# Optimization experiments

Hardware: AMD Instinct MI355X
Metric: run time of the kernel (lower is better)

Reference implementation:

```python
import jax, jax.numpy as jnp
import numpy as np
from jax import lax

OBS_LEN = 8
PRED_LEN = 12
DIM = 128      # hidden_dim
EMB = 64       # embedding_dim
HEADS = 4
MODES = 5
SCENE = 32     # peds per scene
NPED = 8192    # total peds (256 scenes)


def _lin(key, out_d, in_d):
    kw, kb = jax.random.split(key)
    w = jax.random.normal(kw, (out_d, in_d), jnp.float32) / np.sqrt(in_d).astype(np.float32)
    b = jax.random.normal(kb, (out_d,), jnp.float32) * 0.01
    return w, b


def _stack(key, n, out_d, in_d):
    ws, bs = zip(*[_lin(k, out_d, in_d) for k in jax.random.split(key, n)])
    return jnp.stack(ws), jnp.stack(bs)


def setup_inputs() -> dict:
    key = jax.random.key(0)
    ks = jax.random.split(key, 24)
    inp = {}
    inp['obs_traj'] = jax.random.normal(ks[0], (OBS_LEN, NPED, 2), jnp.float32)
    inp['pe_w'], inp['pe_b'] = _lin(ks[1], EMB, 2)
    inp['lstm_wih'], inp['lstm_bih'] = _lin(ks[2], 4 * DIM, EMB)
    inp['lstm_whh'], inp['lstm_bhh'] = _lin(ks[3], 4 * DIM, DIM)
    inp['rp_w1'], inp['rp_b1'] = _lin(ks[4], DIM // 2, 2)
    inp['rp_w2'], inp['rp_b2'] = _lin(ks[5], DIM, DIM // 2)
    inp['wq'], inp['bq'] = _lin(ks[6], DIM, DIM)
    inp['wk'], inp['bk'] = _lin(ks[7], DIM, DIM)
    inp['wv'], inp['bv'] = _lin(ks[8], DIM, DIM)
    inp['wo'], inp['bo'] = _lin(ks[9], DIM, DIM)
    inp['op_w'], inp['op_b'] = _lin(ks[10], DIM, 2 * DIM)
    inp['mp_w1'], inp['mp_b1'] = _lin(ks[11], DIM, 2 * DIM)
    inp['mp_w2'], inp['mp_b2'] = _lin(ks[12], MODES, DIM)
    inp['td_w1'], inp['td_b1'] = _stack(ks[13], MODES, DIM, 2 * DIM)
    inp['td_w2'], inp['td_b2'] = _stack(ks[14], MODES, DIM, DIM)
    inp['td_w3'], inp['td_b3'] = _stack(ks[15], MODES, PRED_LEN * 2, DIM)
    inp['ud_w1'], inp['ud_b1'] = _stack(ks[16], MODES, DIM // 2, 2 * DIM)
    inp['ud_w2'], inp['ud_b2'] = _stack(ks[17], MODES, PRED_LEN * 2, DIM // 2)
    inp['scene_size'] = SCENE
    return inp


def reference(obs_traj, pe_w, pe_b, lstm_wih, lstm_bih, lstm_whh, lstm_bhh,
              rp_w1, rp_b1, rp_w2, rp_b2, wq, bq, wk, bk, wv, bv, wo, bo,
              op_w, op_b, mp_w1, mp_b1, mp_w2, mp_b2,
              td_w1, td_b1, td_w2, td_b2, td_w3, td_b3,
              ud_w1, ud_b1, ud_w2, ud_b2, scene_size):
    obs = jnp.transpose(obs_traj, (1, 0, 2))          # (N, T, 2)
    N = obs.shape[0]
    D = lstm_whh.shape[1]

    # ---- NodeHistoryEncoder: Linear embed + 1-layer LSTM, last hidden ----
    emb = jnp.einsum('ntd,ed->nte', obs, pe_w) + pe_b  # (N, T, EMB)

    def step(carry, x):
        h, c = carry
        g = x @ lstm_wih.T + lstm_bih + h @ lstm_whh.T + lstm_bhh
        i, f, gg, o = jnp.split(g, 4, axis=-1)          # torch gate order i,f,g,o
        c = jax.nn.sigmoid(f) * c + jax.nn.sigmoid(i) * jnp.tanh(gg)
        h = jax.nn.sigmoid(o) * jnp.tanh(c)
        return (h, c), None

    h0 = jnp.zeros((N, D), obs.dtype)
    (node_features, _), _ = lax.scan(step, (h0, h0), jnp.swapaxes(emb, 0, 1))
    last_pos = obs[:, -1, :]                            # (N, 2)

    # ---- EdgeEncoder: per-scene rel-pos-biased multi-head attention ----
    S = scene_size
    B = N // S
    feat = node_features.reshape(B, S, D)
    pos = last_pos.reshape(B, S, 2)
    rel = pos[:, None, :, :] - pos[:, :, None, :]       # [b,i,j] = pos_j - pos_i
    rel_enc = jax.nn.relu(jnp.einsum('bijd,hd->bijh', rel, rp_w1) + rp_b1)
    rel_enc = jnp.einsum('bijh,eh->bije', rel_enc, rp_w2) + rp_b2  # (B,S,S,D)
    kv = feat[:, None, :, :] + rel_enc                  # key == value
    dh = D // HEADS
    q = (feat @ wq.T + bq).reshape(B, S, HEADS, dh)
    kp = (jnp.einsum('bijd,ed->bije', kv, wk) + bk).reshape(B, S, S, HEADS, dh)
    vp = (jnp.einsum('bijd,ed->bije', kv, wv) + bv).reshape(B, S, S, HEADS, dh)
    scores = jnp.einsum('bihd,bijhd->bhij', q, kp) / np.sqrt(dh).astype(np.float32)
    attn = jax.nn.softmax(scores, axis=-1)
    ctx = jnp.einsum('bhij,bijhd->bihd', attn, vp).reshape(B, S, D)
    attn_out = ctx @ wo.T + bo
    edge = (jnp.concatenate([feat, attn_out], axis=-1) @ op_w.T + op_b).reshape(N, D)

    f_all = jnp.concatenate([node_features, edge], axis=-1)  # (N, 2D)

    # ---- GMMDecoder ----
    probs = jax.nn.softmax(jax.nn.relu(f_all @ mp_w1.T + mp_b1) @ mp_w2.T + mp_b2, axis=-1)
    h1 = jax.nn.relu(jnp.einsum('nd,mhd->nmh', f_all, td_w1) + td_b1)    # (N,M,D)
    h2 = jax.nn.relu(jnp.einsum('nmh,mgh->nmg', h1, td_w2) + td_b2)
    traj = (jnp.einsum('nmg,mog->nmo', h2, td_w3) + td_b3).reshape(N, MODES, PRED_LEN, 2)
    u1 = jax.nn.relu(jnp.einsum('nd,mhd->nmh', f_all, ud_w1) + ud_b1)
    sigmas = jax.nn.softplus(jnp.einsum('nmh,moh->nmo', u1, ud_w2) + ud_b2).reshape(N, MODES, PRED_LEN, 2)
    predictions = jnp.cumsum(traj, axis=2) + last_pos[:, None, None, :]
    return predictions, probs
```

## Files before the change

### kernel.cpp

```cpp
#include <hip/hip_runtime.h>
#include <math.h>

typedef __attribute__((ext_vector_type(8))) short short8;
typedef __attribute__((ext_vector_type(4))) float f32x4;

#define NPED 8192
#define INVS 0.1767766952966369f

#define B_WHH    0
#define B_WQKV   131072
#define B_WK2PAD 229376
#define B_OPWE   294912
#define B_MPW1   360448
#define B_TDW1   425984
#define B_TDW2   753664
#define B_TDW3C  917504
#define F_WIHE   958464
#define F_BEFF   962560
#define F_WV2T   964608
#define F_BQKV   997376
#define F_BEDGE  998912
#define F_TDB3C  999424
#define F_ZERO   999936
#define A_FEAT   1000960
#define A_QKV    3098112

__device__ __forceinline__ float bf2f(ushort u) {
  union { unsigned i; float f; } v; v.i = ((unsigned)u) << 16; return v.f;
}
__device__ __forceinline__ float blo(unsigned u) {
  union { unsigned i; float f; } v; v.i = u << 16; return v.f;
}
__device__ __forceinline__ float bhi(unsigned u) {
  union { unsigned i; float f; } v; v.i = u & 0xffff0000u; return v.f;
}
__device__ __forceinline__ ushort f2bf(float f) {
  union { float f; unsigned i; } v; v.f = f;
  unsigned r = v.i + 0x7fffu + ((v.i >> 16) & 1u);
  return (ushort)(r >> 16);
}

__global__ __launch_bounds__(256) void prep(
    const float* __restrict__ wih, const float* __restrict__ bih, const float* __restrict__ bhh,
    const float* __restrict__ pew, const float* __restrict__ peb,
    const float* __restrict__ wk, const float* __restrict__ wv,
    const float* __restrict__ rpw2, const float* __restrict__ rpb2,
    const float* __restrict__ bq, const float* __restrict__ bk, const float* __restrict__ bv,
    const float* __restrict__ whh, const float* __restrict__ wq, const float* __restrict__ wo,
    const float* __restrict__ opw, const float* __restrict__ opb, const float* __restrict__ bo,
    const float* __restrict__ mpw1,
    const float* __restrict__ tdw1, const float* __restrict__ tdw2,
    const float* __restrict__ tdw3, const float* __restrict__ tdb3,
    char* __restrict__ wsb) {
  int tid = blockIdx.x * 256 + threadIdx.x;
  if (tid < 512) {
    int d = tid;
    float s0 = 0.f, s1 = 0.f, sb = 0.f;
    for (int e = 0; e < 64; ++e) {
      float w = wih[d * 64 + e];
      s0 += w * pew[e * 2]; s1 += w * pew[e * 2 + 1]; sb += w * peb[e];
    }
    ((float*)(wsb + F_WIHE))[d * 2] = s0;
    ((float*)(wsb + F_WIHE))[d * 2 + 1] = s1;
    ((float*)(wsb + F_BEFF))[d] = bih[d] + bhh[d] + sb;
  } else if (tid < 49664) {
    int j = tid - 512; int n = j >> 7, k = j & 127;
    float v = (n < 128) ? wq[n * 128 + k] * INVS
                        : (n < 256) ? wk[(n - 128) * 128 + k] : wv[(n - 256) * 128 + k];
    ((ushort*)(wsb + B_WQKV))[j] = f2bf(v);
  } else if (tid < 82432) {
    int idx = tid - 49664; int r = idx >> 7, d = idx & 127;
    int h = r >> 6, e = r & 63;
    float s = 0.f;
    if ((d >> 5) == h)
      for (int c = 0; c < 128; ++c) s += wk[d * 128 + c] * rpw2[c * 64 + e];
    ((ushort*)(wsb + B_WK2PAD))[idx] = f2bf(s);
  } else if (tid < 115200) {
    int idx = tid - 82432; int o = idx >> 8, k = idx & 255;
    float s;
    if (k < 128) s = opw[o * 256 + k];
    else {
      s = 0.f;
      for (int c = 0; c < 128; ++c) s += opw[o * 256 + 128 + c] * wo[c * 128 + (k - 128)];
    }
    ((ushort*)(wsb + B_OPWE))[idx] = f2bf(s);
  } else if (tid < 147968) {
    int j = tid - 115200; ((ushort*)(wsb + B_MPW1))[j] = f2bf(mpw1[j]);
  } else if (tid < 311808) {
    int j = tid - 147968; ((ushort*)(wsb + B_TDW1))[j] = f2bf(tdw1[j]);
  } else if (tid < 393728) {
    int j = tid - 311808; ((ushort*)(wsb + B_TDW2))[j] = f2bf(tdw2[j]);
  } else if (tid < 414208) {
    int j = tid - 393728; int m = j >> 12, r = j & 4095, o = r >> 7, k = r & 127;
    float s = 0.f;
    if (o < 24) {
      int c = o & 1, jj = o >> 1;
      for (int jp = 0; jp <= jj; ++jp) s += tdw3[(m * 24 + jp * 2 + c) * 128 + k];
    }
    ((ushort*)(wsb + B_TDW3C))[j] = f2bf(s);
  } else if (tid < 414328) {
    int j = tid - 414208; int m = j / 24, o = j % 24;
    int c = o & 1, jj = o >> 1;
    float s = 0.f;
    for (int jp = 0; jp <= jj; ++jp) s += tdb3[m * 24 + jp * 2 + c];
    ((float*)(wsb + F_TDB3C))[j] = s;
  } else if (tid < 414712) {
    int d = tid - 414328;
    float s;
    if (d < 128) s = bq[d] * INVS;
    else if (d < 256) {
      int dd = d - 128; s = bk[dd];
      for (int c = 0; c < 128; ++c) s += wk[dd * 128 + c] * rpb2[c];
    } else {
      int dd = d - 256; s = bv[dd];
      for (int c = 0; c < 128; ++c) s += wv[dd * 128 + c] * rpb2[c];
    }
    ((float*)(wsb + F_BQKV))[d] = s;
  } else if (tid < 414840) {
    int o = tid - 414712;
    float s = opb[o];
    for (int c = 0; c < 128; ++c) s += opw[o * 256 + 128 + c] * bo[c];
    ((float*)(wsb + F_BEDGE))[o] = s;
  } else if (tid < 415096) {
    ((float*)(wsb + F_ZERO))[tid - 414840] = 0.f;
  } else if (tid < 423288) {
    int idx = tid - 415096; int e = idx >> 7, hd = idx & 127;
    float s = 0.f;
    for (int c = 0; c < 128; ++c) s += wv[hd * 128 + c] * rpw2[c * 64 + e];
    ((float*)(wsb + F_WV2T))[idx] = s;
  } else if (tid < 488824) {
    int i = tid - 423288;
    ((ushort*)(wsb + B_WHH))[i] = f2bf(whh[i]);
  }
}

__global__ __launch_bounds__(512) void lstm_mfma(
    const float* __restrict__ obs, const ushort* __restrict__ whhb,
    const float* __restrict__ wihe, const float* __restrict__ beff,
    ushort* __restrict__ feat) {
  __shared__ ushort Hs[32 * 128];
  __shared__ float obs_s[8][32][2];
  int tid = threadIdx.x;
  int w = tid >> 6, l = tid & 63;
  int lm = l & 15, lg = l >> 4;
  int nb = blockIdx.x * 32;
  {
    int ts = tid >> 6, p = (tid >> 1) & 31, c = tid & 1;
    obs_s[ts][p][c] = obs[ts * (NPED * 2) + (nb + p) * 2 + c];
  }
  for (int i = tid; i < 4096; i += 512) Hs[i] = 0;
  short8 bfr[4][4];
  float wx0[4], wx1[4], be[4];
#pragma unroll
  for (int q = 0; q < 4; ++q) {
    int g = q * 128 + w * 16 + lm;
    wx0[q] = wihe[g * 2]; wx1[q] = wihe[g * 2 + 1]; be[q] = beff[g];
#pragma unroll
    for (int ks = 0; ks < 4; ++ks)
      bfr[q][ks] = *(const short8*)(const void*)&whhb[g * 128 + ks * 32 + lg * 8];
  }
  float cst[2][4] = {};
  __syncthreads();
  for (int ts = 0; ts < 8; ++ts) {
    f32x4 acc[2][4];
#pragma unroll
    for (int mi = 0; mi < 2; ++mi)
#pragma unroll
      for (int r = 0; r < 4; ++r) {
        int p = mi * 16 + lg * 4 + r;
        float ox = obs_s[ts][p][0], oy = obs_s[ts][p][1];
#pragma unroll
        for (int q = 0; q < 4; ++q)
          acc[mi][q][r] = be[q] + wx0[q] * ox + wx1[q] * oy;
      }
#pragma unroll
    for (int ks = 0; ks < 4; ++ks) {
      int p0 = lm, p1 = 16 + lm;
      short8 a0 = *(const short8*)(const void*)&Hs[p0 * 128 + ((ks * 32 + lg * 8) ^ ((p0 & 7) << 3))];
      short8 a1 = *(const short8*)(const void*)&Hs[p1 * 128 + ((ks * 32 + lg * 8) ^ ((p1 & 7) << 3))];
#pragma unroll
      for (int q = 0; q < 4; ++q) {
        acc[0][q] = __builtin_amdgcn_mfma_f32_16x16x32_bf16(a0, bfr[q][ks], acc[0][q], 0, 0, 0);
        acc[1][q] = __builtin_amdgcn_mfma_f32_16x16x32_bf16(a1, bfr[q][ks], acc[1][q], 0, 0, 0);
      }
    }
    __syncthreads();
    int d = w * 16 + lm;
#pragma unroll
    for (int mi = 0; mi < 2; ++mi)
#pragma unroll
      for (int r = 0; r < 4; ++r) {
        int p = mi * 16 + lg * 4 + r;
        float xi = acc[mi][0][r], xf = acc[mi][1][r], xg = acc[mi][2][r], xo = acc[mi][3][r];
        float ig = 1.f / (1.f + __expf(-xi));
        float fg = 1.f / (1.f + __expf(-xf));
        xg = fminf(fmaxf(xg, -30.f), 30.f);
        float eg = __expf(-2.f * xg);
        float gg = (1.f - eg) / (1.f + eg);
        float og = 1.f / (1.f + __expf(-xo));
        float cv = fg * cst[mi][r] + ig * gg;
        cst[mi][r] = cv;
        float cvc = fminf(fmaxf(cv, -30.f), 30.f);
        float ec = __expf(-2.f * cvc);
        float th = (1.f - ec) / (1.f + ec);
        ushort hb = f2bf(og * th);
        Hs[p * 128 + (d ^ ((p & 7) << 3))] = hb;
        if (ts == 7) feat[(size_t)(nb + p) * 128 + d] = hb;
      }
    __syncthreads();
  }
}

template<int NF, int NKS, int K1KS>
__global__ __launch_bounds__(256) void mfma_gemm(
    const ushort* __restrict__ A1, int lda1,
    const ushort* __restrict__ A2, int lda2,
    const ushort* __restrict__ Bw,
    const float* __restrict__ bias,
    ushort* __restrict__ out, int ldo, int ooff, int relu) {
  int w = threadIdx.x >> 6, l = threadIdx.x & 63;
  int lm = l & 15, lg = l >> 4;
  int row = blockIdx.x * 64 + w * 16 + lm;
  int col0 = blockIdx.y * (NF * 16);
  f32x4 acc[NF];
#pragma unroll
  for (int i = 0; i < NF; ++i) acc[i] = (f32x4){0.f, 0.f, 0.f, 0.f};
#pragma unroll
  for (int ks = 0; ks < NKS; ++ks) {
    int kb = ks * 32 + lg * 8;
    const ushort* ap = (ks < K1KS) ? (A1 + (size_t)row * lda1 + kb)
                                   : (A2 + (size_t)row * lda2 + (kb - K1KS * 32));
    short8 af = *(const short8*)(const void*)ap;
#pragma unroll
    for (int ni = 0; ni < NF; ++ni) {
      short8 bf = *(const short8*)(const void*)(Bw + (size_t)(col0 + ni * 16 + lm) * (NKS * 32) + kb);
      acc[ni] = __builtin_amdgcn_mfma_f32_16x16x32_bf16(af, bf, acc[ni], 0, 0, 0);
    }
  }
  int orow0 = blockIdx.x * 64 + w * 16 + lg * 4;
#pragma unroll
  for (int ni = 0; ni < NF; ++ni) {
    int c = col0 + ni * 16 + lm;
    float bv = bias[c];
#pragma unroll
    for (int r = 0; r < 4; ++r) {
      float v = acc[ni][r] + bv;
      if (relu) v = fmaxf(v, 0.f);
      out[(size_t)(orow0 + r) * ldo + ooff + c] = f2bf(v);
    }
  }
}

__global__ __launch_bounds__(256) void mp_probs(
    const ushort* __restrict__ feat, const ushort* __restrict__ qkv,
    const ushort* __restrict__ w1b, const float* __restrict__ mpb1,
    const float* __restrict__ mpw2, const float* __restrict__ mpb2,
    float* __restrict__ out) {
  __shared__ float w2s[5][128];
  int t = threadIdx.x;
  for (int i = t; i < 640; i += 256) w2s[i >> 7][i & 127] = mpw2[i];
  __syncthreads();
  int w = t >> 6, l = t & 63, lm = l & 15, lg = l >> 4;
  int row = blockIdx.x * 64 + w * 16 + lm;
  f32x4 acc[8];
#pragma unroll
  for (int i = 0; i < 8; ++i) acc[i] = (f32x4){0.f, 0.f, 0.f, 0.f};
#pragma unroll
  for (int ks = 0; ks < 8; ++ks) {
    int kb = ks * 32 + lg * 8;
    const ushort* ap = (ks < 4) ? (feat + (size_t)row * 128 + kb)
                                : (qkv + (size_t)row * 640 + 256 + (kb - 128));
    short8 af = *(const short8*)(const void*)ap;
#pragma unroll
    for (int ni = 0; ni < 8; ++ni) {
      short8 bf = *(const short8*)(const void*)(w1b + (size_t)(ni * 16 + lm) * 256 + kb);
      acc[ni] = __builtin_amdgcn_mfma_f32_16x16x32_bf16(af, bf, acc[ni], 0, 0, 0);
    }
  }
  float bc[8];
#pragma unroll
  for (int ni = 0; ni < 8; ++ni) bc[ni] = mpb1[ni * 16 + lm];
  float lgt[4][5];
#pragma unroll
  for (int r = 0; r < 4; ++r)
#pragma unroll
    for (int m = 0; m < 5; ++m) {
      float s = 0.f;
#pragma unroll
      for (int ni = 0; ni < 8; ++ni)
        s += fmaxf(acc[ni][r] + bc[ni], 0.f) * w2s[m][ni * 16 + lm];
      lgt[r][m] = s;
    }
#pragma unroll
  for (int mask = 1; mask < 16; mask <<= 1)
#pragma unroll
    for (int r = 0; r < 4; ++r)
#pragma unroll
      for (int m = 0; m < 5; ++m)
        lgt[r][m] += __shfl_xor(lgt[r][m], mask);
  if (lm < 5) {
#pragma unroll
    for (int r = 0; r < 4; ++r) {
      float b0 = lgt[r][0] + mpb2[0];
      float mx = b0;
      float lv[5]; lv[0] = b0;
#pragma unroll
      for (int m = 1; m < 5; ++m) { lv[m] = lgt[r][m] + mpb2[m]; mx = fmaxf(mx, lv[m]); }
      float sm = 0.f;
#pragma unroll
      for (int m = 0; m < 5; ++m) { lv[m] = expf(lv[m] - mx); sm += lv[m]; }
      int n = blockIdx.x * 64 + w * 16 + lg * 4 + r;
      out[983040 + (size_t)n * 5 + lm] = lv[lm] / sm;
    }
  }
}

__global__ __launch_bounds__(256) void td_fused(
    const ushort* __restrict__ feat, const ushort* __restrict__ qkv,
    const ushort* __restrict__ w1b, const float* __restrict__ tdb1,
    const ushort* __restrict__ w2b, const float* __restrict__ tdb2,
    const ushort* __restrict__ w3c, const float* __restrict__ b3c,
    const float* __restrict__ obs, float* __restrict__ out) {
  __shared__ ushort slab[64 * 136];
  int t = threadIdx.x, w = t >> 6, l = t & 63, lm = l & 15, lg = l >> 4;
  int m = blockIdx.y;
  int row = blockIdx.x * 64 + w * 16 + lm;
  const ushort* W1 = w1b + (size_t)m * 32768;
  const ushort* W2 = w2b + (size_t)m * 16384;
  const ushort* W3 = w3c + (size_t)m * 4096;
  const float* B1 = tdb1 + m * 128;
  const float* B2 = tdb2 + m * 128;
  f32x4 a1[8];
#pragma unroll
  for (int i = 0; i < 8; ++i) a1[i] = (f32x4){0.f, 0.f, 0.f, 0.f};
#pragma unroll
  for (int ks = 0; ks < 8; ++ks) {
    int kb = ks * 32 + lg * 8;
    const ushort* ap = (ks < 4) ? (feat + (size_t)row * 128 + kb)
                                : (qkv + (size_t)row * 640 + 256 + (kb - 128));
    short8 af = *(const short8*)(const void*)ap;
#pragma unroll
    for (int ni = 0; ni < 8; ++ni) {
      short8 bf = *(const short8*)(const void*)(W1 + (size_t)(ni * 16 + lm) * 256 + kb);
      a1[ni] = __builtin_amdgcn_mfma_f32_16x16x32_bf16(af, bf, a1[ni], 0, 0, 0);
    }
  }
#pragma unroll
  for (int ni = 0; ni < 8; ++ni) {
    float bb = B1[ni * 16 + lm];
#pragma unroll
    for (int r = 0; r < 4; ++r)
      slab[(w * 16 + lg * 4 + r) * 136 + ni * 16 + lm] = f2bf(fmaxf(a1[ni][r] + bb, 0.f));
  }
  __syncthreads();
  short8 af2[4];
#pragma unroll
  for (int ks = 0; ks < 4; ++ks)
    af2[ks] = *(const short8*)(const void*)&slab[(w * 16 + lm) * 136 + ks * 32 + lg * 8];
  f32x4 a2[8];
#pragma unroll
  for (int i = 0; i < 8; ++i) a2[i] = (f32x4){0.f, 0.f, 0.f, 0.f};
#pragma unroll
  for (int ks = 0; ks < 4; ++ks) {
    int kb = ks * 32 + lg * 8;
#pragma unroll
    for (int ni = 0; ni < 8; ++ni) {
      short8 bf = *(const short8*)(const void*)(W2 + (size_t)(ni * 16 + lm) * 128 + kb);
      a2[ni] = __builtin_amdgcn_mfma_f32_16x16x32_bf16(af2[ks], bf, a2[ni], 0, 0, 0);
    }
  }
  __syncthreads();
#pragma unroll
  for (int ni = 0; ni < 8; ++ni) {
    float bb = B2[ni * 16 + lm];
#pragma unroll
    for (int r = 0; r < 4; ++r)
      slab[(w * 16 + lg * 4 + r) * 136 + ni * 16 + lm] = f2bf(fmaxf(a2[ni][r] + bb, 0.f));
  }
  __syncthreads();
  short8 af3[4];
#pragma unroll
  for (int ks = 0; ks < 4; ++ks)
    af3[ks] = *(const short8*)(const void*)&slab[(w * 16 + lm) * 136 + ks * 32 + lg * 8];
  f32x4 a3[2];
  a3[0] = (f32x4){0.f, 0.f, 0.f, 0.f}; a3[1] = (f32x4){0.f, 0.f, 0.f, 0.f};
#pragma unroll
  for (int ks = 0; ks < 4; ++ks) {
    int kb = ks * 32 + lg * 8;
#pragma unroll
    for (int ni = 0; ni < 2; ++ni) {
      short8 bf = *(const short8*)(const void*)(W3 + (size_t)(ni * 16 + lm) * 128 + kb);
      a3[ni] = __builtin_amdgcn_mfma_f32_16x16x32_bf16(af3[ks], bf, a3[ni], 0, 0, 0);
    }
  }
#pragma unroll
  for (int ni = 0; ni < 2; ++ni) {
    int o = ni * 16 + lm;
    if (o < 24) {
      float bb = b3c[m * 24 + o];
      int c = o & 1;
#pragma unroll
      for (int r = 0; r < 4; ++r) {
        int n = blockIdx.x * 64 + w * 16 + lg * 4 + r;
        out[(size_t)n * 120 + m * 24 + o] = a3[ni][r] + bb + obs[7 * (NPED * 2) + n * 2 + c];
      }
    }
  }
}

__global__ __launch_bounds__(256) void attn_kernel(
    const float* __restrict__ obs, ushort* QKV,
    const float* __restrict__ wv2T,
    const float* __restrict__ rpw1, const float* __restrict__ rpb1) {
  __shared__ ushort K0s[32 * 128];
  __shared__ ushort V0s[32 * 128];
  __shared__ ushort renc[4 * 32 * 64];
  __shared__ float Qi[4][128];
  __shared__ float QWs[4][256];
  __shared__ float att[4][4][32];
  __shared__ float AR[4][4][64];
  __shared__ float rpx[64], rpy[64], rpb[64];
  __shared__ float posS[32][2];
  __shared__ float posI[4][2];
  int t = threadIdx.x;
  int scene = blockIdx.x & 255, ic = blockIdx.x >> 8;
  int i0 = ic * 4, sbase = scene * 32;

  for (int idx = t; idx < 1024; idx += 256) {
    int arr = idx >> 9, j = (idx >> 4) & 31, c = idx & 15;
    short8 v = *(const short8*)(const void*)&QKV[(size_t)(sbase + j) * 640 + 128 + arr * 128 + c * 8];
    ushort* dst = arr ? V0s : K0s;
    *(short8*)(void*)&dst[j * 128 + (c ^ (j & 7)) * 8] = v;
  }
  for (int idx = t; idx < 512; idx += 256) {
    int ii = idx >> 7, d = idx & 127;
    Qi[ii][d] = bf2f(QKV[(size_t)(sbase + i0 + ii) * 640 + d]);
  }
  for (int idx = t; idx < 1024; idx += 256) {
    int ii = idx >> 8, e = idx & 255;
    QWs[ii][e] = bf2f(QKV[(size_t)(sbase + i0 + ii) * 640 + 384 + e]);
  }
  if (t < 64) posS[t >> 1][t & 1] = obs[7 * (NPED * 2) + (sbase + (t >> 1)) * 2 + (t & 1)];
  else if (t < 72) {
    int q = t - 64;
    posI[q >> 1][q & 1] = obs[7 * (NPED * 2) + (sbase + i0 + (q >> 1)) * 2 + (q & 1)];
  } else if (t >= 128 && t < 192) {
    int e = t - 128;
    rpx[e] = rpw1[e * 2]; rpy[e] = rpw1[e * 2 + 1]; rpb[e] = rpb1[e];
  }
  __syncthreads();

  for (int idx = t; idx < 1024; idx += 256) {
    int ii = idx >> 8, j = (idx >> 3) & 31, c = idx & 7;
    float dx = posS[j][0] - posI[ii][0], dy = posS[j][1] - posI[ii][1];
    short8 pk;
#pragma unroll
    for (int r = 0; r < 8; ++r) {
      int e = c * 8 + r;
      pk[r] = (short)f2bf(fmaxf(rpx[e] * dx + rpy[e] * dy + rpb[e], 0.f));
    }
    *(short8*)(void*)&renc[(ii * 32 + j) * 64 + (c ^ (j & 7)) * 8] = pk;
  }
  __syncthreads();

  for (int idx = t; idx < 512; idx += 256) {
    int ii = idx >> 7, h = (idx >> 5) & 3, j = idx & 31;
    float s = 0.f;
#pragma unroll
    for (int cc = 0; cc < 4; ++cc) {
      uint4 kv = *(const uint4*)(const void*)&K0s[j * 128 + (((h * 4 + cc) ^ (j & 7)) * 8)];
      const float4 qa = *(const float4*)&Qi[ii][h * 32 + cc * 8];
      const float4 qb = *(const float4*)&Qi[ii][h * 32 + cc * 8 + 4];
      s += blo(kv.x) * qa.x + bhi(kv.x) * qa.y + blo(kv.y) * qa.z + bhi(kv.y) * qa.w;
      s += blo(kv.z) * qb.x + bhi(kv.z) * qb.y + blo(kv.w) * qb.z + bhi(kv.w) * qb.w;
    }
#pragma unroll
    for (int c = 0; c < 8; ++c) {
      uint4 rv = *(const uint4*)(const void*)&renc[(ii * 32 + j) * 64 + ((c ^ (j & 7)) * 8)];
      const float4 ua = *(const float4*)&QWs[ii][h * 64 + c * 8];
      const float4 ub = *(const float4*)&QWs[ii][h * 64 + c * 8 + 4];
      s += blo(rv.x) * ua.x + bhi(rv.x) * ua.y + blo(rv.y) * ua.z + bhi(rv.y) * ua.w;
      s += blo(rv.z) * ub.x + bhi(rv.z) * ub.y + blo(rv.w) * ub.z + bhi(rv.w) * ub.w;
    }
    att[ii][h][j] = s;
  }
  __syncthreads();

  {
    int r = t >> 4, lj = t & 15;
    float v0 = att[r >> 2][r & 3][lj], v1 = att[r >> 2][r & 3][lj + 16];
    float mx = fmaxf(v0, v1);
    mx = fmaxf(mx, __shfl_xor(mx, 8, 16));
    mx = fmaxf(mx, __shfl_xor(mx, 4, 16));
    mx = fmaxf(mx, __shfl_xor(mx, 2, 16));
    mx = fmaxf(mx, __shfl_xor(mx, 1, 16));
    float e0 = expf(v0 - mx), e1 = expf(v1 - mx);
    float sm = e0 + e1;
    sm += __shfl_xor(sm, 8, 16);
    sm += __shfl_xor(sm, 4, 16);
    sm += __shfl_xor(sm, 2, 16);
    sm += __shfl_xor(sm, 1, 16);
    float inv = 1.f / sm;
    att[r >> 2][r & 3][lj] = e0 * inv;
    att[r >> 2][r & 3][lj + 16] = e1 * inv;
  }
  __syncthreads();

  {
    int ii = t >> 6, h = (t >> 4) & 3, e4 = t & 15;
    int c = e4 >> 1, off = (e4 & 1) * 4;
    float a0 = 0.f, a1 = 0.f, a2 = 0.f, a3 = 0.f;
    for (int j = 0; j < 32; ++j) {
      float av = att[ii][h][j];
      uint2 rv = *(const uint2*)(const void*)&renc[(ii * 32 + j) * 64 + ((c ^ (j & 7)) * 8) + off];
      a0 += av * blo(rv.x); a1 += av * bhi(rv.x);
      a2 += av * blo(rv.y); a3 += av * bhi(rv.y);
    }
    *(float4*)&AR[ii][h][e4 * 4] = make_float4(a0, a1, a2, a3);
  }
  __syncthreads();

  {
    int ii = t >> 6, l = t & 63;
    int h5 = l >> 5, hd4 = l & 31;
    int hd = hd4 * 4, h = hd >> 5;
    float c0 = 0.f, c1 = 0.f, c2 = 0.f, c3 = 0.f;
    int cch = hd >> 3, offh = hd & 7;
    for (int j = h5 * 16; j < h5 * 16 + 16; ++j) {
      float av = att[ii][h][j];
      uint2 vv = *(const uint2*)(const void*)&V0s[j * 128 + ((cch ^ (j & 7)) * 8) + offh];
      c0 += av * blo(vv.x); c1 += av * bhi(vv.x);
      c2 += av * blo(vv.y); c3 += av * bhi(vv.y);
    }
    for (int e4 = h5 * 8; e4 < h5 * 8 + 8; ++e4) {
      const float4 ar = *(const float4*)&AR[ii][h][e4 * 4];
#pragma unroll
      for (int r = 0; r < 4; ++r) {
        const float4 wv = *(const float4*)&wv2T[(e4 * 4 + r) * 128 + hd];
        float a = (r == 0) ? ar.x : (r == 1) ? ar.y : (r == 2) ? ar.z : ar.w;
        c0 += a * wv.x; c1 += a * wv.y; c2 += a * wv.z; c3 += a * wv.w;
      }
    }
    c0 += __shfl_xor(c0, 32); c1 += __shfl_xor(c1, 32);
    c2 += __shfl_xor(c2, 32); c3 += __shfl_xor(c3, 32);
    if (h5 == 0) {
      ushort4 o;
      o.x = f2bf(c0); o.y = f2bf(c1); o.z = f2bf(c2); o.w = f2bf(c3);
      *(ushort4*)(void*)&QKV[(size_t)(sbase + i0 + ii) * 640 + hd] = o;
    }
  }
}

extern "C" void kernel_launch(void* const* d_in, const int* in_sizes, int n_in,
                              void* d_out, int out_size, void* d_ws, size_t ws_size,
                              hipStream_t stream) {
  (void)in_sizes; (void)n_in; (void)out_size; (void)ws_size;
  const float* obs  = (const float*)d_in[0];
  const float* pew  = (const float*)d_in[1];
  const float* peb  = (const float*)d_in[2];
  const float* wih  = (const float*)d_in[3];
  const float* bih  = (const float*)d_in[4];
  const float* whh  = (const float*)d_in[5];
  const float* bhh  = (const float*)d_in[6];
  const float* rpw1 = (const float*)d_in[7];
  const float* rpb1 = (const float*)d_in[8];
  const float* rpw2 = (const float*)d_in[9];
  const float* rpb2 = (const float*)d_in[10];
  const float* wq   = (const float*)d_in[11];
  const float* bq   = (const float*)d_in[12];
  const float* wk   = (const float*)d_in[13];
  const float* bk   = (const float*)d_in[14];
  const float* wv   = (const float*)d_in[15];
  const float* bv   = (const float*)d_in[16];
  const float* wo   = (const float*)d_in[17];
  const float* bo   = (const float*)d_in[18];
  const float* opw  = (const float*)d_in[19];
  const float* opb  = (const float*)d_in[20];
  const float* mpw1 = (const float*)d_in[21];
  const float* mpb1 = (const float*)d_in[22];
  const float* mpw2 = (const float*)d_in[23];
  const float* mpb2 = (const float*)d_in[24];
  const float* tdw1 = (const float*)d_in[25];
  const float* tdb1 = (const float*)d_in[26];
  const float* tdw2 = (const float*)d_in[27];
  const float* tdb2 = (const float*)d_in[28];
  const float* tdw3 = (const float*)d_in[29];
  const float* tdb3 = (const float*)d_in[30];
  char* wsb = (char*)d_ws;
  float* out = (float*)d_out;

  ushort* whhb   = (ushort*)(wsb + B_WHH);
  ushort* wqkvb  = (ushort*)(wsb + B_WQKV);
  ushort* wk2pb  = (ushort*)(wsb + B_WK2PAD);
  ushort* opweb  = (ushort*)(wsb + B_OPWE);
  ushort* mpw1b  = (ushort*)(wsb + B_MPW1);
  ushort* tdw1b  = (ushort*)(wsb + B_TDW1);
  ushort* tdw2b  = (ushort*)(wsb + B_TDW2);
  ushort* tdw3cb = (ushort*)(wsb + B_TDW3C);
  ushort* featb  = (ushort*)(wsb + A_FEAT);
  ushort* qkvb   = (ushort*)(wsb + A_QKV);

  prep<<<1910, 256, 0, stream>>>(wih, bih, bhh, pew, peb, wk, wv, rpw2, rpb2,
                                 bq, bk, bv, whh, wq, wo, opw, opb, bo, mpw1,
                                 tdw1, tdw2, tdw3, tdb3, wsb);
  lstm_mfma<<<256, 512, 0, stream>>>(obs, whhb, (float*)(wsb + F_WIHE),
                                     (float*)(wsb + F_BEFF), featb);
  mfma_gemm<4, 4, 4><<<dim3(128, 6), 256, 0, stream>>>(
      featb, 128, featb, 128, wqkvb, (float*)(wsb + F_BQKV), qkvb, 640, 0, 0);
  mfma_gemm<4, 4, 4><<<dim3(128, 4), 256, 0, stream>>>(
      qkvb, 640, qkvb, 640, wk2pb, (float*)(wsb + F_ZERO), qkvb, 640, 384, 0);
  attn_kernel<<<2048, 256, 0, stream>>>(obs, qkvb, (float*)(wsb + F_WV2T), rpw1, rpb1);
  mfma_gemm<4, 8, 4><<<dim3(128, 2), 256, 0, stream>>>(
      featb, 128, qkvb, 640, opweb, (float*)(wsb + F_BEDGE), qkvb, 640, 256, 0);
  mp_probs<<<128, 256, 0, stream>>>(featb, qkvb, mpw1b, mpb1, mpw2, mpb2, out);
  td_fused<<<dim3(128, 5), 256, 0, stream>>>(featb, qkvb, tdw1b, tdb1, tdw2b, tdb2,
                                             tdw3cb, (float*)(wsb + F_TDB3C), obs, out);
}
```

Baseline: 276.4 us.

## Fold K-projection into QKV weights, fuse mode-prob into trajectory decoder, halve row tiles

New measurement: 265.5 us. 1.04x faster.

```diff
diff --git a/kernel.cpp b/kernel.cpp
--- a/kernel.cpp
+++ b/kernel.cpp
@@ -9,21 +9,20 @@
 
 #define B_WHH    0
 #define B_WQKV   131072
-#define B_WK2PAD 229376
-#define B_OPWE   294912
-#define B_MPW1   360448
-#define B_TDW1   425984
-#define B_TDW2   753664
-#define B_TDW3C  917504
-#define F_WIHE   958464
-#define F_BEFF   962560
-#define F_WV2T   964608
-#define F_BQKV   997376
-#define F_BEDGE  998912
-#define F_TDB3C  999424
-#define F_ZERO   999936
-#define A_FEAT   1000960
-#define A_QKV    3098112
+#define B_WK2PAD 294912
+#define B_OPWE   360448
+#define B_MPW1   425984
+#define B_TDW1   491520
+#define B_TDW2   819200
+#define B_TDW3C  983040
+#define F_WIHE   1024000
+#define F_BEFF   1028096
+#define F_WV2T   1030144
+#define F_BQKV   1062912
+#define F_BEDGE  1065472
+#define F_TDB3C  1065984
+#define A_FEAT   1066496
+#define A_QKV    3163648
 
 __device__ __forceinline__ float bf2f(ushort u) {
   union { unsigned i; float f; } v; v.i = ((unsigned)u) << 16; return v.f;
@@ -104,25 +103,23 @@
     float s = 0.f;
     for (int jp = 0; jp <= jj; ++jp) s += tdb3[m * 24 + jp * 2 + c];
     ((float*)(wsb + F_TDB3C))[j] = s;
-  } else if (tid < 414712) {
+  } else if (tid < 414968) {
     int d = tid - 414328;
-    float s;
+    float s = 0.f;
     if (d < 128) s = bq[d] * INVS;
     else if (d < 256) {
       int dd = d - 128; s = bk[dd];
       for (int c = 0; c < 128; ++c) s += wk[dd * 128 + c] * rpb2[c];
-    } else {
+    } else if (d < 384) {
       int dd = d - 256; s = bv[dd];
       for (int c = 0; c < 128; ++c) s += wv[dd * 128 + c] * rpb2[c];
     }
     ((float*)(wsb + F_BQKV))[d] = s;
-  } else if (tid < 414840) {
-    int o = tid - 414712;
+  } else if (tid < 415096) {
+    int o = tid - 414968;
     float s = opb[o];
     for (int c = 0; c < 128; ++c) s += opw[o * 256 + 128 + c] * bo[c];
     ((float*)(wsb + F_BEDGE))[o] = s;
-  } else if (tid < 415096) {
-    ((float*)(wsb + F_ZERO))[tid - 414840] = 0.f;
   } else if (tid < 423288) {
     int idx = tid - 415096; int e = idx >> 7, hd = idx & 127;
     float s = 0.f;
@@ -131,6 +128,29 @@
   } else if (tid < 488824) {
     int i = tid - 423288;
     ((ushort*)(wsb + B_WHH))[i] = f2bf(whh[i]);
+  }
+}
+
+__global__ __launch_bounds__(256) void prep2(
+    const ushort* __restrict__ wk2pad, const float* __restrict__ wq,
+    const float* __restrict__ bq, ushort* __restrict__ wqkv, float* __restrict__ bqkv) {
+  int idx = blockIdx.x * 256 + threadIdx.x;
+  if (idx < 32768) {
+    int e = idx >> 7, k = idx & 127, h = e >> 6;
+    float s = 0.f;
+    for (int dd = 0; dd < 32; ++dd) {
+      int d = h * 32 + dd;
+      s += bf2f(wk2pad[e * 128 + d]) * wq[d * 128 + k];
+    }
+    wqkv[(384 + e) * 128 + k] = f2bf(s * INVS);
+  } else if (idx < 33024) {
+    int e = idx - 32768, h = e >> 6;
+    float s = 0.f;
+    for (int dd = 0; dd < 32; ++dd) {
+      int d = h * 32 + dd;
+      s += bf2f(wk2pad[e * 128 + d]) * bq[d];
+    }
+    bqkv[384 + e] = s * INVS;
   }
 }
 
@@ -211,7 +231,7 @@
   }
 }
 
-template<int NF, int NKS, int K1KS>
+template<int NF, int NKS, int K1KS, int RS>
 __global__ __launch_bounds__(256) void mfma_gemm(
     const ushort* __restrict__ A1, int lda1,
     const ushort* __restrict__ A2, int lda2,
@@ -220,8 +240,16 @@
     ushort* __restrict__ out, int ldo, int ooff, int relu) {
   int w = threadIdx.x >> 6, l = threadIdx.x & 63;
   int lm = l & 15, lg = l >> 4;
-  int row = blockIdx.x * 64 + w * 16 + lm;
-  int col0 = blockIdx.y * (NF * 16);
+  int row, col0, orow0;
+  if (RS) {
+    row = blockIdx.x * 32 + (w >> 1) * 16 + lm;
+    col0 = blockIdx.y * (NF * 32) + (w & 1) * (NF * 16);
+    orow0 = blockIdx.x * 32 + (w >> 1) * 16 + lg * 4;
+  } else {
+    row = blockIdx.x * 64 + w * 16 + lm;
+    col0 = blockIdx.y * (NF * 16);
+    orow0 = blockIdx.x * 64 + w * 16 + lg * 4;
+  }
   f32x4 acc[NF];
 #pragma unroll
   for (int i = 0; i < NF; ++i) acc[i] = (f32x4){0.f, 0.f, 0.f, 0.f};
@@ -237,7 +265,6 @@
       acc[ni] = __builtin_amdgcn_mfma_f32_16x16x32_bf16(af, bf, acc[ni], 0, 0, 0);
     }
   }
-  int orow0 = blockIdx.x * 64 + w * 16 + lg * 4;
 #pragma unroll
   for (int ni = 0; ni < NF; ++ni) {
     int c = col0 + ni * 16 + lm;
@@ -251,158 +278,159 @@
   }
 }
 
-__global__ __launch_bounds__(256) void mp_probs(
-    const ushort* __restrict__ feat, const ushort* __restrict__ qkv,
-    const ushort* __restrict__ w1b, const float* __restrict__ mpb1,
-    const float* __restrict__ mpw2, const float* __restrict__ mpb2,
-    float* __restrict__ out) {
-  __shared__ float w2s[5][128];
-  int t = threadIdx.x;
-  for (int i = t; i < 640; i += 256) w2s[i >> 7][i & 127] = mpw2[i];
-  __syncthreads();
-  int w = t >> 6, l = t & 63, lm = l & 15, lg = l >> 4;
-  int row = blockIdx.x * 64 + w * 16 + lm;
-  f32x4 acc[8];
-#pragma unroll
-  for (int i = 0; i < 8; ++i) acc[i] = (f32x4){0.f, 0.f, 0.f, 0.f};
-#pragma unroll
-  for (int ks = 0; ks < 8; ++ks) {
-    int kb = ks * 32 + lg * 8;
-    const ushort* ap = (ks < 4) ? (feat + (size_t)row * 128 + kb)
-                                : (qkv + (size_t)row * 640 + 256 + (kb - 128));
-    short8 af = *(const short8*)(const void*)ap;
-#pragma unroll
-    for (int ni = 0; ni < 8; ++ni) {
-      short8 bf = *(const short8*)(const void*)(w1b + (size_t)(ni * 16 + lm) * 256 + kb);
-      acc[ni] = __builtin_amdgcn_mfma_f32_16x16x32_bf16(af, bf, acc[ni], 0, 0, 0);
-    }
-  }
-  float bc[8];
-#pragma unroll
-  for (int ni = 0; ni < 8; ++ni) bc[ni] = mpb1[ni * 16 + lm];
-  float lgt[4][5];
-#pragma unroll
-  for (int r = 0; r < 4; ++r)
-#pragma unroll
-    for (int m = 0; m < 5; ++m) {
-      float s = 0.f;
-#pragma unroll
-      for (int ni = 0; ni < 8; ++ni)
-        s += fmaxf(acc[ni][r] + bc[ni], 0.f) * w2s[m][ni * 16 + lm];
-      lgt[r][m] = s;
-    }
-#pragma unroll
-  for (int mask = 1; mask < 16; mask <<= 1)
-#pragma unroll
-    for (int r = 0; r < 4; ++r)
-#pragma unroll
-      for (int m = 0; m < 5; ++m)
-        lgt[r][m] += __shfl_xor(lgt[r][m], mask);
-  if (lm < 5) {
-#pragma unroll
-    for (int r = 0; r < 4; ++r) {
-      float b0 = lgt[r][0] + mpb2[0];
-      float mx = b0;
-      float lv[5]; lv[0] = b0;
-#pragma unroll
-      for (int m = 1; m < 5; ++m) { lv[m] = lgt[r][m] + mpb2[m]; mx = fmaxf(mx, lv[m]); }
-      float sm = 0.f;
-#pragma unroll
-      for (int m = 0; m < 5; ++m) { lv[m] = expf(lv[m] - mx); sm += lv[m]; }
-      int n = blockIdx.x * 64 + w * 16 + lg * 4 + r;
-      out[983040 + (size_t)n * 5 + lm] = lv[lm] / sm;
-    }
-  }
-}
-
-__global__ __launch_bounds__(256) void td_fused(
+__global__ __launch_bounds__(256) void td_mp(
     const ushort* __restrict__ feat, const ushort* __restrict__ qkv,
     const ushort* __restrict__ w1b, const float* __restrict__ tdb1,
     const ushort* __restrict__ w2b, const float* __restrict__ tdb2,
     const ushort* __restrict__ w3c, const float* __restrict__ b3c,
+    const float* __restrict__ mpw1b, const float* __restrict__ mpb1,
+    const float* __restrict__ mpw2, const float* __restrict__ mpb2,
     const float* __restrict__ obs, float* __restrict__ out) {
-  __shared__ ushort slab[64 * 136];
+  __shared__ float smem[32 * 72];
   int t = threadIdx.x, w = t >> 6, l = t & 63, lm = l & 15, lg = l >> 4;
-  int m = blockIdx.y;
-  int row = blockIdx.x * 64 + w * 16 + lm;
-  const ushort* W1 = w1b + (size_t)m * 32768;
-  const ushort* W2 = w2b + (size_t)m * 16384;
-  const ushort* W3 = w3c + (size_t)m * 4096;
-  const float* B1 = tdb1 + m * 128;
-  const float* B2 = tdb2 + m * 128;
-  f32x4 a1[8];
-#pragma unroll
-  for (int i = 0; i < 8; ++i) a1[i] = (f32x4){0.f, 0.f, 0.f, 0.f};
-#pragma unroll
-  for (int ks = 0; ks < 8; ++ks) {
-    int kb = ks * 32 + lg * 8;
-    const ushort* ap = (ks < 4) ? (feat + (size_t)row * 128 + kb)
-                                : (qkv + (size_t)row * 640 + 256 + (kb - 128));
-    short8 af = *(const short8*)(const void*)ap;
-#pragma unroll
-    for (int ni = 0; ni < 8; ++ni) {
-      short8 bf = *(const short8*)(const void*)(W1 + (size_t)(ni * 16 + lm) * 256 + kb);
-      a1[ni] = __builtin_amdgcn_mfma_f32_16x16x32_bf16(af, bf, a1[ni], 0, 0, 0);
-    }
-  }
-#pragma unroll
-  for (int ni = 0; ni < 8; ++ni) {
-    float bb = B1[ni * 16 + lm];
-#pragma unroll
-    for (int r = 0; r < 4; ++r)
-      slab[(w * 16 + lg * 4 + r) * 136 + ni * 16 + lm] = f2bf(fmaxf(a1[ni][r] + bb, 0.f));
-  }
-  __syncthreads();
-  short8 af2[4];
-#pragma unroll
-  for (int ks = 0; ks < 4; ++ks)
-    af2[ks] = *(const short8*)(const void*)&slab[(w * 16 + lm) * 136 + ks * 32 + lg * 8];
-  f32x4 a2[8];
-#pragma unroll
-  for (int i = 0; i < 8; ++i) a2[i] = (f32x4){0.f, 0.f, 0.f, 0.f};
-#pragma unroll
-  for (int ks = 0; ks < 4; ++ks) {
-    int kb = ks * 32 + lg * 8;
-#pragma unroll
-    for (int ni = 0; ni < 8; ++ni) {
-      short8 bf = *(const short8*)(const void*)(W2 + (size_t)(ni * 16 + lm) * 128 + kb);
-      a2[ni] = __builtin_amdgcn_mfma_f32_16x16x32_bf16(af2[ks], bf, a2[ni], 0, 0, 0);
-    }
-  }
-  __syncthreads();
-#pragma unroll
-  for (int ni = 0; ni < 8; ++ni) {
-    float bb = B2[ni * 16 + lm];
-#pragma unroll
-    for (int r = 0; r < 4; ++r)
-      slab[(w * 16 + lg * 4 + r) * 136 + ni * 16 + lm] = f2bf(fmaxf(a2[ni][r] + bb, 0.f));
-  }
-  __syncthreads();
-  short8 af3[4];
-#pragma unroll
-  for (int ks = 0; ks < 4; ++ks)
-    af3[ks] = *(const short8*)(const void*)&slab[(w * 16 + lm) * 136 + ks * 32 + lg * 8];
-  f32x4 a3[2];
-  a3[0] = (f32x4){0.f, 0.f, 0.f, 0.f}; a3[1] = (f32x4){0.f, 0.f, 0.f, 0.f};
-#pragma unroll
-  for (int ks = 0; ks < 4; ++ks) {
-    int kb = ks * 32 + lg * 8;
-#pragma unroll
-    for (int ni = 0; ni < 2; ++ni) {
-      short8 bf = *(const short8*)(const void*)(W3 + (size_t)(ni * 16 + lm) * 128 + kb);
-      a3[ni] = __builtin_amdgcn_mfma_f32_16x16x32_bf16(af3[ks], bf, a3[ni], 0, 0, 0);
-    }
-  }
-#pragma unroll
-  for (int ni = 0; ni < 2; ++ni) {
-    int o = ni * 16 + lm;
+  int wr = w >> 1, wc = w & 1;
+  int z = blockIdx.y;
+
+  if (z < 5) {
+    ushort* slab = (ushort*)smem;
+    int m = z;
+    int row = blockIdx.x * 32 + wr * 16 + lm;
+    const ushort* W1 = w1b + (size_t)m * 32768;
+    const ushort* W2 = w2b + (size_t)m * 16384;
+    const ushort* W3 = w3c + (size_t)m * 4096;
+    const float* B1 = tdb1 + m * 128;
+    const float* B2 = tdb2 + m * 128;
+    f32x4 a1[4];
+#pragma unroll
+    for (int i = 0; i < 4; ++i) a1[i] = (f32x4){0.f, 0.f, 0.f, 0.f};
+#pragma unroll
+    for (int ks = 0; ks < 8; ++ks) {
+      int kb = ks * 32 + lg * 8;
+      const ushort* ap = (ks < 4) ? (feat + (size_t)row * 128 + kb)
+                                  : (qkv + (size_t)row * 640 + 256 + (kb - 128));
+      short8 af = *(const short8*)(const void*)ap;
+#pragma unroll
+      for (int ni = 0; ni < 4; ++ni) {
+        short8 bf = *(const short8*)(const void*)(W1 + (size_t)(wc * 64 + ni * 16 + lm) * 256 + kb);
+        a1[ni] = __builtin_amdgcn_mfma_f32_16x16x32_bf16(af, bf, a1[ni], 0, 0, 0);
+      }
+    }
+#pragma unroll
+    for (int ni = 0; ni < 4; ++ni) {
+      int c = wc * 64 + ni * 16 + lm;
+      float bb = B1[c];
+#pragma unroll
+      for (int r = 0; r < 4; ++r)
+        slab[(wr * 16 + lg * 4 + r) * 136 + c] = f2bf(fmaxf(a1[ni][r] + bb, 0.f));
+    }
+    __syncthreads();
+    short8 af2[4];
+#pragma unroll
+    for (int ks = 0; ks < 4; ++ks)
+      af2[ks] = *(const short8*)(const void*)&slab[(wr * 16 + lm) * 136 + ks * 32 + lg * 8];
+    f32x4 a2[4];
+#pragma unroll
+    for (int i = 0; i < 4; ++i) a2[i] = (f32x4){0.f, 0.f, 0.f, 0.f};
+#pragma unroll
+    for (int ks = 0; ks < 4; ++ks) {
+      int kb = ks * 32 + lg * 8;
+#pragma unroll
+      for (int ni = 0; ni < 4; ++ni) {
+        short8 bf = *(const short8*)(const void*)(W2 + (size_t)(wc * 64 + ni * 16 + lm) * 128 + kb);
+        a2[ni] = __builtin_amdgcn_mfma_f32_16x16x32_bf16(af2[ks], bf, a2[ni], 0, 0, 0);
+      }
+    }
+    __syncthreads();
+#pragma unroll
+    for (int ni = 0; ni < 4; ++ni) {
+      int c = wc * 64 + ni * 16 + lm;
+      float bb = B2[c];
+#pragma unroll
+      for (int r = 0; r < 4; ++r)
+        slab[(wr * 16 + lg * 4 + r) * 136 + c] = f2bf(fmaxf(a2[ni][r] + bb, 0.f));
+    }
+    __syncthreads();
+    short8 af3[4], w3f[4];
+#pragma unroll
+    for (int ks = 0; ks < 4; ++ks) {
+      af3[ks] = *(const short8*)(const void*)&slab[(wr * 16 + lm) * 136 + ks * 32 + lg * 8];
+      w3f[ks] = *(const short8*)(const void*)(W3 + (size_t)(wc * 16 + lm) * 128 + ks * 32 + lg * 8);
+    }
+    f32x4 a3 = (f32x4){0.f, 0.f, 0.f, 0.f};
+#pragma unroll
+    for (int ks = 0; ks < 4; ++ks)
+      a3 = __builtin_amdgcn_mfma_f32_16x16x32_bf16(af3[ks], w3f[ks], a3, 0, 0, 0);
+    int o = wc * 16 + lm;
     if (o < 24) {
       float bb = b3c[m * 24 + o];
       int c = o & 1;
 #pragma unroll
       for (int r = 0; r < 4; ++r) {
-        int n = blockIdx.x * 64 + w * 16 + lg * 4 + r;
-        out[(size_t)n * 120 + m * 24 + o] = a3[ni][r] + bb + obs[7 * (NPED * 2) + n * 2 + c];
+        int n = blockIdx.x * 32 + wr * 16 + lg * 4 + r;
+        out[(size_t)n * 120 + m * 24 + o] = a3[r] + bb + obs[7 * (NPED * 2) + n * 2 + c];
+      }
+    }
+  } else {
+    float* w2s = smem;
+    float* pc  = smem + 640;
+    for (int i = t; i < 640; i += 256) w2s[(i >> 7) * 128 + (i & 127)] = mpw2[i];
+    int g = wr, ch = wc, cb = ch * 64;
+    int row = blockIdx.x * 32 + g * 16 + lm;
+    f32x4 acc[4];
+#pragma unroll
+    for (int i = 0; i < 4; ++i) acc[i] = (f32x4){0.f, 0.f, 0.f, 0.f};
+#pragma unroll
+    for (int ks = 0; ks < 8; ++ks) {
+      int kb = ks * 32 + lg * 8;
+      const ushort* ap = (ks < 4) ? (feat + (size_t)row * 128 + kb)
+                                  : (qkv + (size_t)row * 640 + 256 + (kb - 128));
+      short8 af = *(const short8*)(const void*)ap;
+#pragma unroll
+      for (int ni = 0; ni < 4; ++ni) {
+        short8 bf = *(const short8*)(const void*)((const ushort*)mpw1b + (size_t)(cb + ni * 16 + lm) * 256 + kb);
+        acc[ni] = __builtin_amdgcn_mfma_f32_16x16x32_bf16(af, bf, acc[ni], 0, 0, 0);
+      }
+    }
+    __syncthreads();
+    float bc[4];
+#pragma unroll
+    for (int ni = 0; ni < 4; ++ni) bc[ni] = mpb1[cb + ni * 16 + lm];
+    float lgt[4][5];
+#pragma unroll
+    for (int r = 0; r < 4; ++r)
+#pragma unroll
+      for (int m = 0; m < 5; ++m) {
+        float s = 0.f;
+#pragma unroll
+        for (int ni = 0; ni < 4; ++ni)
+          s += fmaxf(acc[ni][r] + bc[ni], 0.f) * w2s[m * 128 + cb + ni * 16 + lm];
+        lgt[r][m] = s;
+      }
+#pragma unroll
+    for (int mask = 1; mask < 16; mask <<= 1)
+#pragma unroll
+      for (int r = 0; r < 4; ++r)
+#pragma unroll
+        for (int m = 0; m < 5; ++m)
+          lgt[r][m] += __shfl_xor(lgt[r][m], mask);
+    if (ch == 1 && lm < 5) {
+#pragma unroll
+      for (int r = 0; r < 4; ++r) pc[(g * 16 + lg * 4 + r) * 5 + lm] = lgt[r][lm];
+    }
+    __syncthreads();
+    if (ch == 0 && lm < 5) {
+#pragma unroll
+      for (int r = 0; r < 4; ++r) {
+        float lv[5], mx = -1e30f, sm = 0.f;
+#pragma unroll
+        for (int m = 0; m < 5; ++m) {
+          lv[m] = lgt[r][m] + pc[(g * 16 + lg * 4 + r) * 5 + m] + mpb2[m];
+          mx = fmaxf(mx, lv[m]);
+        }
+#pragma unroll
+        for (int m = 0; m < 5; ++m) { lv[m] = expf(lv[m] - mx); sm += lv[m]; }
+        int n = blockIdx.x * 32 + g * 16 + lg * 4 + r;
+        out[983040 + (size_t)n * 5 + lm] = lv[lm] / sm;
       }
     }
   }
@@ -603,16 +631,15 @@
   prep<<<1910, 256, 0, stream>>>(wih, bih, bhh, pew, peb, wk, wv, rpw2, rpb2,
                                  bq, bk, bv, whh, wq, wo, opw, opb, bo, mpw1,
                                  tdw1, tdw2, tdw3, tdb3, wsb);
+  prep2<<<129, 256, 0, stream>>>(wk2pb, wq, bq, wqkvb, (float*)(wsb + F_BQKV));
   lstm_mfma<<<256, 512, 0, stream>>>(obs, whhb, (float*)(wsb + F_WIHE),
                                      (float*)(wsb + F_BEFF), featb);
-  mfma_gemm<4, 4, 4><<<dim3(128, 6), 256, 0, stream>>>(
+  mfma_gemm<4, 4, 4, 0><<<dim3(128, 10), 256, 0, stream>>>(
       featb, 128, featb, 128, wqkvb, (float*)(wsb + F_BQKV), qkvb, 640, 0, 0);
-  mfma_gemm<4, 4, 4><<<dim3(128, 4), 256, 0, stream>>>(
-      qkvb, 640, qkvb, 640, wk2pb, (float*)(wsb + F_ZERO), qkvb, 640, 384, 0);
   attn_kernel<<<2048, 256, 0, stream>>>(obs, qkvb, (float*)(wsb + F_WV2T), rpw1, rpb1);
-  mfma_gemm<4, 8, 4><<<dim3(128, 2), 256, 0, stream>>>(
+  mfma_gemm<2, 8, 4, 1><<<dim3(256, 2), 256, 0, stream>>>(
       featb, 128, qkvb, 640, opweb, (float*)(wsb + F_BEDGE), qkvb, 640, 256, 0);
-  mp_probs<<<128, 256, 0, stream>>>(featb, qkvb, mpw1b, mpb1, mpw2, mpb2, out);
-  td_fused<<<dim3(128, 5), 256, 0, stream>>>(featb, qkvb, tdw1b, tdb1, tdw2b, tdb2,
-                                             tdw3cb, (float*)(wsb + F_TDB3C), obs, out);
-}
+  td_mp<<<dim3(256, 6), 256, 0, stream>>>(featb, qkvb, tdw1b, tdb1, tdw2b, tdb2,
+                                          tdw3cb, (float*)(wsb + F_TDB3C),
+                                          (const float*)mpw1b, mpb1, mpw2, mpb2, obs, out);
+}
```
